# Kernel optimization log

Measured on AMD Instinct MI355X. Metric: run time of the kernel, lower is better.

Reference implementation:

```python
import jax, jax.numpy as jnp
import numpy as np
import math

PHI = (1.0 + math.sqrt(5.0)) / 2.0
LN_EPS = 1e-5


def _carrier_phases(n_heads: int) -> np.ndarray:
    """Reproduce DimensionalHeadManager._allocate carrier phases."""
    base = [k * math.pi / 7.0 for k in range(7)]  # rung base phases
    n_rungs = 7
    raw = []
    remaining = n_heads
    for i in range(n_rungs):
        if i < n_rungs - 1:
            c = max(1, round(n_heads / PHI ** (i + 1)))
            c = min(c, remaining - (n_rungs - 1 - i))
            raw.append(c)
            remaining -= c
        else:
            raw.append(max(1, remaining))
    phases = []
    for rung_idx, count in enumerate(raw):
        for j in range(count):
            phases.append(base[rung_idx] + 2.0 * math.pi / max(count, 1) * j)
    return np.asarray(phases[:n_heads], dtype=np.float32)


def setup_inputs() -> dict:
    key = jax.random.key(0)
    ks = jax.random.split(key, 7)
    B, S, D, H = 2, 2048, 1024, 16
    w_scale = 0.02  # realistic init scale for Linear weights
    x = jax.random.normal(ks[0], (B, S, D), dtype=jnp.float32)
    Wq = jax.random.normal(ks[1], (D, D), dtype=jnp.float32) * w_scale
    Wk = jax.random.normal(ks[2], (D, D), dtype=jnp.float32) * w_scale
    Wv = jax.random.normal(ks[3], (D, D), dtype=jnp.float32) * w_scale
    Wo = jax.random.normal(ks[4], (D, D), dtype=jnp.float32) * w_scale
    Wp = jax.random.normal(ks[5], (D,), dtype=jnp.float32) * w_scale  # W_phase (1,D) flattened
    gamma = jnp.ones((D,), dtype=jnp.float32)
    beta = jnp.zeros((D,), dtype=jnp.float32)
    carrier = jnp.asarray(_carrier_phases(H))  # srl.carrier_freq init
    lam = jnp.float32(0.1)  # lambda_resonance init
    return {"x": x, "Wq": Wq, "Wk": Wk, "Wv": Wv, "Wo": Wo, "Wp": Wp,
            "gamma": gamma, "beta": beta, "carrier": carrier, "lam": lam}


def reference(x, Wq, Wk, Wv, Wo, Wp, gamma, beta, carrier, lam):
    B, S, D = x.shape
    H = carrier.shape[0]
    dh = D // H
    scale = 1.0 / math.sqrt(dh)

    residual = x
    # LayerNorm
    mu = jnp.mean(x, axis=-1, keepdims=True)
    var = jnp.mean((x - mu) ** 2, axis=-1, keepdims=True)
    xn = (x - mu) * jax.lax.rsqrt(var + LN_EPS) * gamma + beta

    # Q/K/V projections (torch Linear: y = x @ W.T), split into heads
    q = jnp.einsum('bsd,ed->bse', xn, Wq).reshape(B, S, H, dh)
    k = jnp.einsum('bsd,ed->bse', xn, Wk).reshape(B, S, H, dh)
    v = jnp.einsum('bsd,ed->bse', xn, Wv).reshape(B, S, H, dh)

    # scalar phase per token, per-head carrier resonance gate
    phase = jnp.einsum('bsd,d->bs', xn, Wp)                       # (B,S)
    head_T = jnp.cos((phase[..., None] - carrier) * 0.5) ** 2     # (B,S,H)

    # attention scores + resonance term R_ij = cos^2((phi_i - phi_j)/2)
    scores = jnp.einsum('bihd,bjhd->bhij', q, k) * scale          # (B,H,S,S)
    R = jnp.cos((phase[:, :, None] - phase[:, None, :]) * 0.5) ** 2  # (B,S,S)
    scores = scores + lam * R[:, None, :, :]

    attn = jax.nn.softmax(scores, axis=-1)
    out = jnp.einsum('bhij,bjhd->bihd', attn, v)                  # (B,S,H,dh)
    out = out * head_T[..., None]                                 # per-head resonance gating
    emergent_energy = jnp.sum(jnp.abs(out))
    y = residual + jnp.einsum('bse,de->bsd', out.reshape(B, S, D), Wo)
    return (y, emergent_energy)
```

## Files before the change

kernel.cpp:

```cpp
#include <hip/hip_runtime.h>
#include <hip/hip_bf16.h>

#define S_LEN 2048
#define D_MODEL 1024
#define NH 16
#define DH 64
#define M_TOK 4096
#define DK 80

typedef __attribute__((ext_vector_type(8))) short bf16x8;
typedef __attribute__((ext_vector_type(4))) float f32x4;
typedef __attribute__((ext_vector_type(16))) float f32x16;

#define LOG2E 1.4426950408889634f

__device__ __forceinline__ unsigned short f2bf(float f) {
  unsigned u = __float_as_uint(f);
  u += 0x7FFF + ((u >> 16) & 1);
  return (unsigned short)(u >> 16);
}

__device__ __forceinline__ void gl16(const void* g, void* l) {
  __builtin_amdgcn_global_load_lds(
      (const __attribute__((address_space(1))) unsigned int*)g,
      (__attribute__((address_space(3))) unsigned int*)l, 16, 0, 0);
}

__device__ __forceinline__ void pl32swap(unsigned int& a, unsigned int& b) {
  asm volatile("v_permlane32_swap_b32 %0, %1" : "+v"(a), "+v"(b));
}

__global__ __launch_bounds__(256) void prep_kernel(
    const float* __restrict__ Wq, const float* __restrict__ Wk,
    const float* __restrict__ Wv, const float* __restrict__ Wo,
    unsigned short* __restrict__ wbf, float* __restrict__ energy) {
  if (blockIdx.x == 0 && threadIdx.x == 0) *energy = 0.f;
  int idx = (blockIdx.x * 256 + threadIdx.x) * 4;
  int wsel = idx >> 20;
  const float* s = (wsel == 0) ? Wq : (wsel == 1) ? Wk : (wsel == 2) ? Wv : Wo;
  int off = idx & 1048575;
  float4 v = *(const float4*)(s + off);
  ushort4 p;
  p.x = f2bf(v.x); p.y = f2bf(v.y); p.z = f2bf(v.z); p.w = f2bf(v.w);
  *(ushort4*)(wbf + idx) = p;
}

__device__ __forceinline__ float block_sum(float v, float* sm) {
#pragma unroll
  for (int o = 32; o > 0; o >>= 1) v += __shfl_xor(v, o, 64);
  int w = threadIdx.x >> 6;
  __syncthreads();
  if ((threadIdx.x & 63) == 0) sm[w] = v;
  __syncthreads();
  return sm[0] + sm[1] + sm[2] + sm[3];
}

__global__ __launch_bounds__(256) void ln_phase_kernel(
    const float* __restrict__ x, const float* __restrict__ Wp,
    const float* __restrict__ gamma, const float* __restrict__ beta,
    unsigned short* __restrict__ xn, float* __restrict__ cosP,
    float* __restrict__ sinP) {
  __shared__ float sm[4];
  int row = blockIdx.x;
  int tid = threadIdx.x;
  float4 v = ((const float4*)(x + (size_t)row * D_MODEL))[tid];
  float mu = block_sum(v.x + v.y + v.z + v.w, sm) * (1.0f / D_MODEL);
  float d0 = v.x - mu, d1 = v.y - mu, d2 = v.z - mu, d3 = v.w - mu;
  float var = block_sum(d0 * d0 + d1 * d1 + d2 * d2 + d3 * d3, sm) * (1.0f / D_MODEL);
  float rinv = rsqrtf(var + 1e-5f);
  float4 g = ((const float4*)gamma)[tid];
  float4 be = ((const float4*)beta)[tid];
  float n0 = d0 * rinv * g.x + be.x;
  float n1 = d1 * rinv * g.y + be.y;
  float n2 = d2 * rinv * g.z + be.z;
  float n3 = d3 * rinv * g.w + be.w;
  ushort4 p;
  p.x = f2bf(n0); p.y = f2bf(n1); p.z = f2bf(n2); p.w = f2bf(n3);
  ((ushort4*)(xn + (size_t)row * D_MODEL))[tid] = p;
  float4 wp = ((const float4*)Wp)[tid];
  float ph = block_sum(n0 * wp.x + n1 * wp.y + n2 * wp.z + n3 * wp.w, sm);
  if (tid == 0) {
    cosP[row] = cosf(ph);
    sinP[row] = sinf(ph);
  }
}

__global__ __launch_bounds__(256) void phase_fill_kernel(
    const float* __restrict__ cosP, const float* __restrict__ sinP,
    unsigned short* __restrict__ kk80) {
  int gid = blockIdx.x * 256 + threadIdx.x;
  int s = gid & (S_LEN - 1);
  int bh = gid >> 11;
  int b = bh >> 4;
  int tok = b * S_LEN + s;
  unsigned int w0 = (unsigned int)f2bf(cosP[tok]) | ((unsigned int)f2bf(sinP[tok]) << 16);
  *(int4*)(kk80 + (size_t)gid * DK + 64) = make_int4((int)w0, 0, 0, 0);
}

__global__ __launch_bounds__(256, 3) void qkv_gemm_kernel(
    const unsigned short* __restrict__ xn, const unsigned short* __restrict__ wbf,
    unsigned short* __restrict__ q, unsigned short* __restrict__ kk80,
    unsigned short* __restrict__ vT) {
  __shared__ __align__(16) unsigned short As[128 * 64];
  __shared__ __align__(16) unsigned short Bs[128 * 64];
  int bid = blockIdx.x;
  bool vmode = bid >= 512;
  const unsigned short* Ap;
  const unsigned short* Bp;
  int m0, n0;
  if (!vmode) {
    m0 = (bid >> 4) * 128;
    n0 = (bid & 15) * 128;
    Ap = xn; Bp = wbf;
  } else {
    int v2 = bid - 512;
    m0 = (v2 & 7) * 128;
    n0 = (v2 >> 3) * 128;
    Ap = wbf + 2 * D_MODEL * D_MODEL; Bp = xn;
  }
  int tid = threadIdx.x;
  int wave = tid >> 6, lane = tid & 63, quad = lane >> 4, l15 = lane & 15;
  int wm = (wave & 1) * 64, wn = (wave >> 1) * 64;
  f32x4 acc[4][4];
#pragma unroll
  for (int r = 0; r < 4; ++r)
#pragma unroll
    for (int c = 0; c < 4; ++c) acc[r][c] = (f32x4){0.f, 0.f, 0.f, 0.f};

  for (int k0 = 0; k0 < D_MODEL; k0 += 64) {
    __syncthreads();
#pragma unroll
    for (int t = 0; t < 4; ++t) {
      int c = t * 256 + tid;
      int r = c >> 3, p = c & 7;
      int g = p ^ (r & 7);
      gl16(&Ap[(size_t)(m0 + r) * D_MODEL + k0 + g * 8], &As[c * 8]);
      gl16(&Bp[(size_t)(n0 + r) * D_MODEL + k0 + g * 8], &Bs[c * 8]);
    }
    __syncthreads();
    bf16x8 af[4][2], bfr[4][2];
#pragma unroll
    for (int r = 0; r < 4; ++r) {
      int R = wm + r * 16 + l15;
#pragma unroll
      for (int h = 0; h < 2; ++h)
        af[r][h] = *(const bf16x8*)&As[R * 64 + ((h * 4 + quad) ^ (R & 7)) * 8];
    }
#pragma unroll
    for (int c = 0; c < 4; ++c) {
      int R = wn + c * 16 + l15;
#pragma unroll
      for (int h = 0; h < 2; ++h)
        bfr[c][h] = *(const bf16x8*)&Bs[R * 64 + ((h * 4 + quad) ^ (R & 7)) * 8];
    }
#pragma unroll
    for (int h = 0; h < 2; ++h)
#pragma unroll
      for (int r = 0; r < 4; ++r)
#pragma unroll
        for (int c = 0; c < 4; ++c)
          acc[r][c] = __builtin_amdgcn_mfma_f32_16x16x32_bf16(af[r][h], bfr[c][h], acc[r][c], 0, 0, 0);
  }
#pragma unroll
  for (int r = 0; r < 4; ++r) {
#pragma unroll
    for (int c = 0; c < 4; ++c) {
#pragma unroll
      for (int rr = 0; rr < 4; ++rr) {
        if (vmode) {
          int e = m0 + wm + r * 16 + quad * 4 + rr;
          int tok = n0 + wn + c * 16 + l15;
          int hh = e >> 6, d = e & 63;
          int bb = tok >> 11, ss = tok & (S_LEN - 1);
          vT[(((size_t)(bb * NH + hh)) * DH + d) * S_LEN + ss] = f2bf(acc[r][c][rr]);
        } else {
          int tok = m0 + wm + r * 16 + quad * 4 + rr;
          int n = n0 + wn + c * 16 + l15;
          int e = n & 1023;
          int hh = e >> 6, d = e & 63;
          int bb = tok >> 11, ss = tok & (S_LEN - 1);
          if ((n0 >> 10) == 0) {
            q[(((size_t)(bb * NH + hh)) * S_LEN + ss) * DH + d] =
                f2bf(acc[r][c][rr] * (0.125f * LOG2E));
          } else {
            kk80[(((size_t)(bb * NH + hh)) * S_LEN + ss) * DK + d] = f2bf(acc[r][c][rr]);
          }
        }
      }
    }
  }
}

__global__ __launch_bounds__(128, 2) void attn_kernel(
    const unsigned short* __restrict__ q, const unsigned short* __restrict__ kk80,
    const unsigned short* __restrict__ vT, const float* __restrict__ cosP,
    const float* __restrict__ sinP, const float* __restrict__ carrier,
    const float* __restrict__ lamp, unsigned short* __restrict__ outw,
    float* __restrict__ energy) {
  __shared__ __align__(16) unsigned short Ks[2][64 * 72];
  __shared__ __align__(16) unsigned short Vs[2][512 * 8];
  __shared__ float Lr[2][32];
  __shared__ float er[2];
  int qt = blockIdx.x, h = blockIdx.y, b = blockIdx.z;
  int bh = b * NH + h;
  int tid = threadIdx.x, wave = tid >> 6, lane = tid & 63;
  int half = lane >> 5, l31 = lane & 31;

  const unsigned short* kb = kk80 + (size_t)bh * S_LEN * DK;
  const unsigned short* vb = vT + (size_t)bh * DH * S_LEN;
  int qrow = qt * 64 + wave * 32 + l31;

  bf16x8 bQ[5];
  {
    const unsigned short* qp = q + ((size_t)bh * S_LEN + qrow) * DH;
#pragma unroll
    for (int db = 0; db < 4; ++db)
      bQ[db] = *(const bf16x8*)(qp + db * 16 + half * 8);
    bf16x8 z8 = {0, 0, 0, 0, 0, 0, 0, 0};
    if (half == 0) {
      float hl2 = 0.5f * lamp[0] * LOG2E;
      z8[0] = (short)f2bf(hl2 * cosP[b * S_LEN + qrow]);
      z8[1] = (short)f2bf(hl2 * sinP[b * S_LEN + qrow]);
    }
    bQ[4] = z8;
  }

  f32x16 O0 = {}, O1 = {};
  float l_i = 0.f;

  auto stage = [&](int bi, int jbase) {
    unsigned short* ksd = &Ks[bi][0];
    unsigned short* vsd = &Vs[bi][0];
#pragma unroll
    for (int t = 0; t < 4; ++t) {
      unsigned int cc = t * 128 + tid;
      unsigned int r = cc / 9u, p = cc - r * 9u;
      gl16(&kb[(size_t)(jbase + r) * DK + p * 8], ksd + cc * 8);
    }
    if (tid < 64) {
      unsigned int cc = 512 + tid;
      unsigned int r = cc / 9u, p = cc - r * 9u;
      gl16(&kb[(size_t)(jbase + r) * DK + p * 8], ksd + cc * 8);
    }
#pragma unroll
    for (int t = 0; t < 4; ++t) {
      int cc = t * 128 + tid;
      int r = cc >> 3, p = cc & 7;
      int g = p ^ (r & 7);
      gl16(&vb[(size_t)r * S_LEN + jbase + g * 8], vsd + cc * 8);
    }
  };

  int cur = 0;
  stage(0, 0);
  __syncthreads();

  for (int jt = 0; jt < 32; ++jt) {
    if (jt < 31) stage(cur ^ 1, (jt + 1) * 64);

    const unsigned short* ksb = &Ks[cur][0];
    const unsigned short* vsb = &Vs[cur][0];

    f32x16 Sf[2];
#pragma unroll
    for (int sj = 0; sj < 2; ++sj) {
      Sf[sj] = (f32x16){};
      int r = sj * 32 + l31;
      __builtin_amdgcn_s_setprio(1);
#pragma unroll
      for (int db = 0; db < 5; ++db) {
        int p = (db < 4) ? (db * 2 + half) : 8;
        bf16x8 aK = *(const bf16x8*)(ksb + (r * 9 + p) * 8);
        Sf[sj] = __builtin_amdgcn_mfma_f32_32x32x16_bf16(aK, bQ[db], Sf[sj], 0, 0, 0);
      }
      __builtin_amdgcn_s_setprio(0);
    }

#pragma unroll
    for (int sj = 0; sj < 2; ++sj) {
      unsigned int w[8];
#pragma unroll
      for (int rr = 0; rr < 8; ++rr) {
        float e0 = exp2f(Sf[sj][rr * 2 + 0]);
        float e1 = exp2f(Sf[sj][rr * 2 + 1]);
        l_i += e0 + e1;
        __hip_bfloat162 pk2 = __float22bfloat162_rn(float2{e0, e1});
        w[rr] = *(unsigned int*)&pk2;
      }
#pragma unroll
      for (int u = 0; u < 2; ++u) {
        unsigned int a0 = w[u * 4 + 0], a1 = w[u * 4 + 1];
        unsigned int b0 = w[u * 4 + 2], b1 = w[u * 4 + 3];
        pl32swap(a0, b0);
        pl32swap(a1, b1);
        union { unsigned int u4[4]; bf16x8 v; } cvt;
        cvt.u4[0] = a0; cvt.u4[1] = a1; cvt.u4[2] = b0; cvt.u4[3] = b1;
        int jb = sj * 2 + u;
        __builtin_amdgcn_s_setprio(1);
        {
          int rv = l31;
          int p = (jb * 2 + half) ^ (rv & 7);
          bf16x8 bV = *(const bf16x8*)(vsb + (rv * 8 + p) * 8);
          O0 = __builtin_amdgcn_mfma_f32_32x32x16_bf16(cvt.v, bV, O0, 0, 0, 0);
        }
        {
          int rv = 32 + l31;
          int p = (jb * 2 + half) ^ (rv & 7);
          bf16x8 bV = *(const bf16x8*)(vsb + (rv * 8 + p) * 8);
          O1 = __builtin_amdgcn_mfma_f32_32x32x16_bf16(cvt.v, bV, O1, 0, 0, 0);
        }
        __builtin_amdgcn_s_setprio(0);
      }
    }

    __syncthreads();
    cur ^= 1;
  }

  l_i += __shfl_xor(l_i, 32, 64);
  Lr[wave][l31] = l_i;
  float ch = cosf(carrier[h]), sh = sinf(carrier[h]);
  float esum = 0.f;
#pragma unroll
  for (int reg = 0; reg < 16; ++reg) {
    int ir = (reg & 3) + 8 * (reg >> 2) + 4 * half;
    int srow = qt * 64 + wave * 32 + ir;
    float cp = cosP[b * S_LEN + srow], sp = sinP[b * S_LEN + srow];
    float gate = 0.5f + 0.5f * (cp * ch + sp * sh);
    float gl = gate / Lr[wave][ir];
    float v0 = O0[reg] * gl, v1 = O1[reg] * gl;
    esum += fabsf(v0) + fabsf(v1);
    size_t tok = (size_t)b * S_LEN + srow;
    outw[tok * D_MODEL + h * DH + l31] = f2bf(v0);
    outw[tok * D_MODEL + h * DH + 32 + l31] = f2bf(v1);
  }
#pragma unroll
  for (int off = 32; off > 0; off >>= 1) esum += __shfl_xor(esum, off, 64);
  if (lane == 0) er[wave] = esum;
  __syncthreads();
  if (tid == 0) atomicAdd(energy, er[0] + er[1]);
}

__global__ __launch_bounds__(256) void out_gemm_kernel(
    const unsigned short* __restrict__ A, const unsigned short* __restrict__ Wo,
    const float* __restrict__ x, float* __restrict__ y) {
  __shared__ __align__(16) unsigned short As[128 * 64];
  __shared__ __align__(16) unsigned short Bs[64 * 64];
  int tid = threadIdx.x;
  int wave = tid >> 6, lane = tid & 63, quad = lane >> 4, l15 = lane & 15;
  int wm = (wave & 1) * 64, wn = (wave >> 1) * 32;
  int m0 = blockIdx.y * 128, n0 = blockIdx.x * 64;
  f32x4 acc[4][2];
#pragma unroll
  for (int r = 0; r < 4; ++r)
#pragma unroll
    for (int c = 0; c < 2; ++c) acc[r][c] = (f32x4){0.f, 0.f, 0.f, 0.f};

  for (int k0 = 0; k0 < D_MODEL; k0 += 64) {
    __syncthreads();
#pragma unroll
    for (int t = 0; t < 4; ++t) {
      int c = t * 256 + tid;
      int r = c >> 3, p = c & 7;
      int qc = p ^ (r & 7);
      gl16(&A[(size_t)(m0 + r) * D_MODEL + k0 + qc * 8], &As[c * 8]);
    }
#pragma unroll
    for (int t = 0; t < 2; ++t) {
      int c = t * 256 + tid;
      int r = c >> 3, p = c & 7;
      int qc = p ^ (r & 7);
      gl16(&Wo[(size_t)(n0 + r) * D_MODEL + k0 + qc * 8], &Bs[c * 8]);
    }
    __syncthreads();
    bf16x8 af[4][2], bfr[2][2];
#pragma unroll
    for (int r = 0; r < 4; ++r) {
      int R = wm + r * 16 + l15;
#pragma unroll
      for (int h = 0; h < 2; ++h)
        af[r][h] = *(const bf16x8*)&As[R * 64 + ((h * 4 + quad) ^ (R & 7)) * 8];
    }
#pragma unroll
    for (int c = 0; c < 2; ++c) {
      int R = wn + c * 16 + l15;
#pragma unroll
      for (int h = 0; h < 2; ++h)
        bfr[c][h] = *(const bf16x8*)&Bs[R * 64 + ((h * 4 + quad) ^ (R & 7)) * 8];
    }
#pragma unroll
    for (int h = 0; h < 2; ++h)
#pragma unroll
      for (int r = 0; r < 4; ++r)
#pragma unroll
        for (int c = 0; c < 2; ++c)
          acc[r][c] = __builtin_amdgcn_mfma_f32_16x16x32_bf16(af[r][h], bfr[c][h], acc[r][c], 0, 0, 0);
  }
#pragma unroll
  for (int r = 0; r < 4; ++r) {
#pragma unroll
    for (int c = 0; c < 2; ++c) {
      int dcol = n0 + wn + c * 16 + l15;
#pragma unroll
      for (int rr = 0; rr < 4; ++rr) {
        int tok = m0 + wm + r * 16 + quad * 4 + rr;
        size_t idx = (size_t)tok * D_MODEL + dcol;
        y[idx] = x[idx] + acc[r][c][rr];
      }
    }
  }
}

extern "C" void kernel_launch(void* const* d_in, const int* in_sizes, int n_in,
                              void* d_out, int out_size, void* d_ws, size_t ws_size,
                              hipStream_t stream) {
  const float* x = (const float*)d_in[0];
  const float* Wq = (const float*)d_in[1];
  const float* Wk = (const float*)d_in[2];
  const float* Wv = (const float*)d_in[3];
  const float* Wo = (const float*)d_in[4];
  const float* Wp = (const float*)d_in[5];
  const float* gamma = (const float*)d_in[6];
  const float* beta = (const float*)d_in[7];
  const float* carrier = (const float*)d_in[8];
  const float* lam = (const float*)d_in[9];

  char* ws = (char*)d_ws;
  const size_t MB = 1024 * 1024;
  unsigned short* wbf = (unsigned short*)(ws);
  unsigned short* xn = (unsigned short*)(ws + 8 * MB);
  unsigned short* qq = (unsigned short*)(ws + 16 * MB);
  unsigned short* kk80 = (unsigned short*)(ws + 24 * MB);
  unsigned short* vT = (unsigned short*)(ws + 34 * MB);
  float* cosP = (float*)(ws + 42 * MB);
  float* sinP = (float*)(ws + 42 * MB + 16 * 1024);
  unsigned short* outw = xn;

  float* y = (float*)d_out;
  float* energy = y + (out_size - 1);

  prep_kernel<<<4096, 256, 0, stream>>>(Wq, Wk, Wv, Wo, wbf, energy);
  ln_phase_kernel<<<M_TOK, 256, 0, stream>>>(x, Wp, gamma, beta, xn, cosP, sinP);
  phase_fill_kernel<<<256, 256, 0, stream>>>(cosP, sinP, kk80);
  qkv_gemm_kernel<<<768, 256, 0, stream>>>(xn, wbf, qq, kk80, vT);
  attn_kernel<<<dim3(32, 16, 2), 128, 0, stream>>>(qq, kk80, vT, cosP, sinP,
                                                   carrier, lam, outw, energy);
  out_gemm_kernel<<<dim3(16, 32), 256, 0, stream>>>(outw, wbf + 3 * D_MODEL * D_MODEL,
                                                    x, y);
}
```

Before: 225.6 us.

## Fuse phase fill into LayerNorm, pipeline attention loads, widen output GEMM tile

Merges the phase-fill kernel into the LayerNorm kernel, which removes one launch. The attention K/V staging now uses precomputed offsets and explicit vmcnt waits with raw barriers, replacing __syncthreads, so loads overlap compute more finely. The energy atomic becomes a per-block partial array that the output GEMM reduces, and the output GEMM tile grows from 128x64 to 128x128 with launch bounds of 3. The changes trade fewer launches and less address arithmetic for higher register pressure in the output GEMM and reliance on the hand-written wait counts being correct.

```diff
diff --git a/kernel.cpp b/kernel.cpp
--- a/kernel.cpp
+++ b/kernel.cpp
@@ -7,6 +7,7 @@
 #define DH 64
 #define M_TOK 4096
 #define DK 80
+#define NT 32
 
 typedef __attribute__((ext_vector_type(8))) short bf16x8;
 typedef __attribute__((ext_vector_type(4))) float f32x4;
@@ -33,8 +34,7 @@
 __global__ __launch_bounds__(256) void prep_kernel(
     const float* __restrict__ Wq, const float* __restrict__ Wk,
     const float* __restrict__ Wv, const float* __restrict__ Wo,
-    unsigned short* __restrict__ wbf, float* __restrict__ energy) {
-  if (blockIdx.x == 0 && threadIdx.x == 0) *energy = 0.f;
+    unsigned short* __restrict__ wbf) {
   int idx = (blockIdx.x * 256 + threadIdx.x) * 4;
   int wsel = idx >> 20;
   const float* s = (wsel == 0) ? Wq : (wsel == 1) ? Wk : (wsel == 2) ? Wv : Wo;
@@ -59,7 +59,7 @@
     const float* __restrict__ x, const float* __restrict__ Wp,
     const float* __restrict__ gamma, const float* __restrict__ beta,
     unsigned short* __restrict__ xn, float* __restrict__ cosP,
-    float* __restrict__ sinP) {
+    float* __restrict__ sinP, unsigned short* __restrict__ kk80) {
   __shared__ float sm[4];
   int row = blockIdx.x;
   int tid = threadIdx.x;
@@ -83,18 +83,13 @@
     cosP[row] = cosf(ph);
     sinP[row] = sinf(ph);
   }
-}
-
-__global__ __launch_bounds__(256) void phase_fill_kernel(
-    const float* __restrict__ cosP, const float* __restrict__ sinP,
-    unsigned short* __restrict__ kk80) {
-  int gid = blockIdx.x * 256 + threadIdx.x;
-  int s = gid & (S_LEN - 1);
-  int bh = gid >> 11;
-  int b = bh >> 4;
-  int tok = b * S_LEN + s;
-  unsigned int w0 = (unsigned int)f2bf(cosP[tok]) | ((unsigned int)f2bf(sinP[tok]) << 16);
-  *(int4*)(kk80 + (size_t)gid * DK + 64) = make_int4((int)w0, 0, 0, 0);
+  if (tid < 16) {
+    float cp = cosf(ph), sp = sinf(ph);
+    unsigned int w0 = (unsigned int)f2bf(cp) | ((unsigned int)f2bf(sp) << 16);
+    int b_ = row >> 11, s_ = row & (S_LEN - 1);
+    *(int4*)(kk80 + ((size_t)((b_ * NH + tid) * S_LEN + s_)) * DK + 64) =
+        make_int4((int)w0, 0, 0, 0);
+  }
 }
 
 __global__ __launch_bounds__(256, 3) void qkv_gemm_kernel(
@@ -196,7 +191,7 @@
     const unsigned short* __restrict__ vT, const float* __restrict__ cosP,
     const float* __restrict__ sinP, const float* __restrict__ carrier,
     const float* __restrict__ lamp, unsigned short* __restrict__ outw,
-    float* __restrict__ energy) {
+    float* __restrict__ earray) {
   __shared__ __align__(16) unsigned short Ks[2][64 * 72];
   __shared__ __align__(16) unsigned short Vs[2][512 * 8];
   __shared__ float Lr[2][32];
@@ -225,41 +220,65 @@
     bQ[4] = z8;
   }
 
+  unsigned int cc0 = tid, cc1 = tid + 128, cc2 = tid + 256, cc3 = tid + 384,
+               cc4 = 512 + (tid & 63);
+  unsigned int kr0 = cc0 / 9u, kr1 = cc1 / 9u, kr2 = cc2 / 9u, kr3 = cc3 / 9u,
+               kr4 = cc4 / 9u;
+  unsigned int ko0 = kr0 * DK + (cc0 - kr0 * 9u) * 8;
+  unsigned int ko1 = kr1 * DK + (cc1 - kr1 * 9u) * 8;
+  unsigned int ko2 = kr2 * DK + (cc2 - kr2 * 9u) * 8;
+  unsigned int ko3 = kr3 * DK + (cc3 - kr3 * 9u) * 8;
+  unsigned int ko4 = kr4 * DK + (cc4 - kr4 * 9u) * 8;
+  unsigned short* kl0 = &Ks[0][0] + cc0 * 8;
+  unsigned short* kl1 = &Ks[0][0] + cc1 * 8;
+  unsigned short* kl2 = &Ks[0][0] + cc2 * 8;
+  unsigned short* kl3 = &Ks[0][0] + cc3 * 8;
+  unsigned short* kl4 = &Ks[0][0] + cc4 * 8;
+  unsigned int vr0 = cc0 >> 3, vr1 = cc1 >> 3, vr2 = cc2 >> 3, vr3 = cc3 >> 3;
+  unsigned int vo0 = vr0 * S_LEN + ((cc0 & 7) ^ (vr0 & 7)) * 8;
+  unsigned int vo1 = vr1 * S_LEN + ((cc1 & 7) ^ (vr1 & 7)) * 8;
+  unsigned int vo2 = vr2 * S_LEN + ((cc2 & 7) ^ (vr2 & 7)) * 8;
+  unsigned int vo3 = vr3 * S_LEN + ((cc3 & 7) ^ (vr3 & 7)) * 8;
+  unsigned short* vl0 = &Vs[0][0] + cc0 * 8;
+  unsigned short* vl1 = &Vs[0][0] + cc1 * 8;
+  unsigned short* vl2 = &Vs[0][0] + cc2 * 8;
+  unsigned short* vl3 = &Vs[0][0] + cc3 * 8;
+
+  const unsigned short* kbt = kb;
+  const unsigned short* vbt = vb;
+
+  auto stage = [&](unsigned int kofs, unsigned int vofs) {
+    gl16(kbt + ko0, kl0 + kofs);
+    gl16(kbt + ko1, kl1 + kofs);
+    gl16(kbt + ko2, kl2 + kofs);
+    gl16(kbt + ko3, kl3 + kofs);
+    gl16(kbt + ko4, kl4 + kofs);
+    gl16(vbt + vo0, vl0 + vofs);
+    gl16(vbt + vo1, vl1 + vofs);
+    gl16(vbt + vo2, vl2 + vofs);
+    gl16(vbt + vo3, vl3 + vofs);
+    kbt += 64 * DK;
+    vbt += 64;
+  };
+
   f32x16 O0 = {}, O1 = {};
   float l_i = 0.f;
 
-  auto stage = [&](int bi, int jbase) {
-    unsigned short* ksd = &Ks[bi][0];
-    unsigned short* vsd = &Vs[bi][0];
-#pragma unroll
-    for (int t = 0; t < 4; ++t) {
-      unsigned int cc = t * 128 + tid;
-      unsigned int r = cc / 9u, p = cc - r * 9u;
-      gl16(&kb[(size_t)(jbase + r) * DK + p * 8], ksd + cc * 8);
-    }
-    if (tid < 64) {
-      unsigned int cc = 512 + tid;
-      unsigned int r = cc / 9u, p = cc - r * 9u;
-      gl16(&kb[(size_t)(jbase + r) * DK + p * 8], ksd + cc * 8);
-    }
-#pragma unroll
-    for (int t = 0; t < 4; ++t) {
-      int cc = t * 128 + tid;
-      int r = cc >> 3, p = cc & 7;
-      int g = p ^ (r & 7);
-      gl16(&vb[(size_t)r * S_LEN + jbase + g * 8], vsd + cc * 8);
-    }
-  };
-
-  int cur = 0;
+  unsigned int kofs = 0, vofs = 0;
   stage(0, 0);
-  __syncthreads();
-
-  for (int jt = 0; jt < 32; ++jt) {
-    if (jt < 31) stage(cur ^ 1, (jt + 1) * 64);
-
-    const unsigned short* ksb = &Ks[cur][0];
-    const unsigned short* vsb = &Vs[cur][0];
+
+  for (int jt = 0; jt < NT; ++jt) {
+    if (jt < NT - 1) {
+      stage(kofs ^ 4608, vofs ^ 4096);
+      asm volatile("s_waitcnt vmcnt(9)" ::: "memory");
+    } else {
+      asm volatile("s_waitcnt vmcnt(0)" ::: "memory");
+    }
+    __builtin_amdgcn_sched_barrier(0);
+    __builtin_amdgcn_s_barrier();
+
+    const unsigned short* ksb = &Ks[0][0] + kofs;
+    const unsigned short* vsb = &Vs[0][0] + vofs;
 
     f32x16 Sf[2];
 #pragma unroll
@@ -313,8 +332,11 @@
       }
     }
 
-    __syncthreads();
-    cur ^= 1;
+    asm volatile("s_waitcnt lgkmcnt(0)" ::: "memory");
+    __builtin_amdgcn_sched_barrier(0);
+    __builtin_amdgcn_s_barrier();
+    kofs ^= 4608;
+    vofs ^= 4096;
   }
 
   l_i += __shfl_xor(l_i, 32, 64);
@@ -338,23 +360,33 @@
   for (int off = 32; off > 0; off >>= 1) esum += __shfl_xor(esum, off, 64);
   if (lane == 0) er[wave] = esum;
   __syncthreads();
-  if (tid == 0) atomicAdd(energy, er[0] + er[1]);
-}
-
-__global__ __launch_bounds__(256) void out_gemm_kernel(
+  if (tid == 0) {
+    int bidl = qt + 32 * (h + NH * b);
+    earray[bidl] = er[0] + er[1];
+  }
+}
+
+__global__ __launch_bounds__(256, 3) void out_gemm_kernel(
     const unsigned short* __restrict__ A, const unsigned short* __restrict__ Wo,
-    const float* __restrict__ x, float* __restrict__ y) {
+    const float* __restrict__ x, const float* __restrict__ earray,
+    float* __restrict__ y, float* __restrict__ energy) {
   __shared__ __align__(16) unsigned short As[128 * 64];
-  __shared__ __align__(16) unsigned short Bs[64 * 64];
+  __shared__ __align__(16) unsigned short Bs[128 * 64];
+  __shared__ float sm[4];
   int tid = threadIdx.x;
+  if (blockIdx.x == 0 && blockIdx.y == 0) {
+    float v = earray[tid] + earray[tid + 256] + earray[tid + 512] + earray[tid + 768];
+    float tot = block_sum(v, sm);
+    if (tid == 0) *energy = tot;
+  }
   int wave = tid >> 6, lane = tid & 63, quad = lane >> 4, l15 = lane & 15;
-  int wm = (wave & 1) * 64, wn = (wave >> 1) * 32;
-  int m0 = blockIdx.y * 128, n0 = blockIdx.x * 64;
-  f32x4 acc[4][2];
+  int wm = (wave & 1) * 64, wn = (wave >> 1) * 64;
+  int m0 = blockIdx.y * 128, n0 = blockIdx.x * 128;
+  f32x4 acc[4][4];
 #pragma unroll
   for (int r = 0; r < 4; ++r)
 #pragma unroll
-    for (int c = 0; c < 2; ++c) acc[r][c] = (f32x4){0.f, 0.f, 0.f, 0.f};
+    for (int c = 0; c < 4; ++c) acc[r][c] = (f32x4){0.f, 0.f, 0.f, 0.f};
 
   for (int k0 = 0; k0 < D_MODEL; k0 += 64) {
     __syncthreads();
@@ -362,18 +394,12 @@
     for (int t = 0; t < 4; ++t) {
       int c = t * 256 + tid;
       int r = c >> 3, p = c & 7;
-      int qc = p ^ (r & 7);
-      gl16(&A[(size_t)(m0 + r) * D_MODEL + k0 + qc * 8], &As[c * 8]);
-    }
-#pragma unroll
-    for (int t = 0; t < 2; ++t) {
-      int c = t * 256 + tid;
-      int r = c >> 3, p = c & 7;
-      int qc = p ^ (r & 7);
-      gl16(&Wo[(size_t)(n0 + r) * D_MODEL + k0 + qc * 8], &Bs[c * 8]);
+      int g = p ^ (r & 7);
+      gl16(&A[(size_t)(m0 + r) * D_MODEL + k0 + g * 8], &As[c * 8]);
+      gl16(&Wo[(size_t)(n0 + r) * D_MODEL + k0 + g * 8], &Bs[c * 8]);
     }
     __syncthreads();
-    bf16x8 af[4][2], bfr[2][2];
+    bf16x8 af[4][2], bfr[4][2];
 #pragma unroll
     for (int r = 0; r < 4; ++r) {
       int R = wm + r * 16 + l15;
@@ -382,7 +408,7 @@
         af[r][h] = *(const bf16x8*)&As[R * 64 + ((h * 4 + quad) ^ (R & 7)) * 8];
     }
 #pragma unroll
-    for (int c = 0; c < 2; ++c) {
+    for (int c = 0; c < 4; ++c) {
       int R = wn + c * 16 + l15;
 #pragma unroll
       for (int h = 0; h < 2; ++h)
@@ -393,13 +419,13 @@
 #pragma unroll
       for (int r = 0; r < 4; ++r)
 #pragma unroll
-        for (int c = 0; c < 2; ++c)
+        for (int c = 0; c < 4; ++c)
           acc[r][c] = __builtin_amdgcn_mfma_f32_16x16x32_bf16(af[r][h], bfr[c][h], acc[r][c], 0, 0, 0);
   }
 #pragma unroll
   for (int r = 0; r < 4; ++r) {
 #pragma unroll
-    for (int c = 0; c < 2; ++c) {
+    for (int c = 0; c < 4; ++c) {
       int dcol = n0 + wn + c * 16 + l15;
 #pragma unroll
       for (int rr = 0; rr < 4; ++rr) {
@@ -434,17 +460,17 @@
   unsigned short* vT = (unsigned short*)(ws + 34 * MB);
   float* cosP = (float*)(ws + 42 * MB);
   float* sinP = (float*)(ws + 42 * MB + 16 * 1024);
+  float* earray = (float*)(ws + 42 * MB + 32 * 1024);
   unsigned short* outw = xn;
 
   float* y = (float*)d_out;
   float* energy = y + (out_size - 1);
 
-  prep_kernel<<<4096, 256, 0, stream>>>(Wq, Wk, Wv, Wo, wbf, energy);
-  ln_phase_kernel<<<M_TOK, 256, 0, stream>>>(x, Wp, gamma, beta, xn, cosP, sinP);
-  phase_fill_kernel<<<256, 256, 0, stream>>>(cosP, sinP, kk80);
+  prep_kernel<<<4096, 256, 0, stream>>>(Wq, Wk, Wv, Wo, wbf);
+  ln_phase_kernel<<<M_TOK, 256, 0, stream>>>(x, Wp, gamma, beta, xn, cosP, sinP, kk80);
   qkv_gemm_kernel<<<768, 256, 0, stream>>>(xn, wbf, qq, kk80, vT);
   attn_kernel<<<dim3(32, 16, 2), 128, 0, stream>>>(qq, kk80, vT, cosP, sinP,
-                                                   carrier, lam, outw, energy);
-  out_gemm_kernel<<<dim3(16, 32), 256, 0, stream>>>(outw, wbf + 3 * D_MODEL * D_MODEL,
-                                                    x, y);
-}
+                                                   carrier, lam, outw, earray);
+  out_gemm_kernel<<<dim3(8, 32), 256, 0, stream>>>(outw, wbf + 3 * D_MODEL * D_MODEL,
+                                                   x, earray, y, energy);
+}
```

Measured after the change: 235.2 us. 1.04x slower.
